# Optimization experiments

Measured on AMD Instinct MI355X. Metric: run time of the kernel, lower is better.

Reference implementation:

```python
import jax, jax.numpy as jnp
import numpy as np

B, T, H, D = 1, 2048, 32, 64
SCALE = 0.015625  # 1/64 = 1/head_size
DEG = 2


def setup_inputs() -> dict:
    key = jax.random.key(0)
    k1, k2, k3, k4 = jax.random.split(key, 4)
    q = jax.random.normal(k1, (B, T, H, D), dtype=jnp.float32)
    k = jax.random.normal(k2, (B, T, H, D), dtype=jnp.float32)
    v = jax.random.normal(k3, (B, T, H, D), dtype=jnp.float32)
    # log_G: per-token, per-head log decay (must be <= 0)
    g = -0.1 * jax.random.uniform(k4, (B, T, H), dtype=jnp.float32)
    return {"q": q, "k": k, "v": v, "g": g}


def reference(q, k, v, g):
    # q,k,v: [B,T,H,D]; g: [B,T,H] log-decay (log_G)
    # Power retention, deg=2, attention (quadratic) form for T <= switch_over_seq_len.
    g_cum = jnp.cumsum(g, axis=1)                         # [B,T,H]
    gc = jnp.transpose(g_cum, (0, 2, 1))                  # [B,H,T]
    # decay weight exp(gc[t]-gc[s]) for s<=t, 0 otherwise
    log_decay = gc[:, :, :, None] - gc[:, :, None, :]     # [B,H,T,S]
    causal = jnp.tril(jnp.ones((T, T), dtype=bool))
    decay = jnp.where(causal, jnp.exp(log_decay), 0.0)    # [B,H,T,S]
    qk = jnp.einsum("bthd,bshd->bhts", q, k) * SCALE      # [B,H,T,S]
    w = (qk ** DEG) * decay                               # nonneg scores, deg=2
    num = jnp.einsum("bhts,bshd->bthd", w, v)             # [B,T,H,D]
    denom = jnp.transpose(w.sum(-1), (0, 2, 1))           # [B,T,H]
    out = num / jnp.maximum(denom, 1.0)[..., None]
    return out
```

## Files before the change

kernel.cpp:

```cpp
#include <hip/hip_runtime.h>

#define T_DIM 2048
#define H_DIM 32
#define D_DIM 64
#define SCALE_F 0.015625f
#define TILE_STRIDE 2048

typedef unsigned short ushort;
typedef __attribute__((ext_vector_type(8))) short short8;
typedef __attribute__((ext_vector_type(16))) float f32x16;
typedef __attribute__((ext_vector_type(2))) float f32x2;
typedef __attribute__((ext_vector_type(4))) float f32x4;

#define MFMA32(A, B, C) __builtin_amdgcn_mfma_f32_32x32x16_bf16((A), (B), (C), 0, 0, 0)

__global__ __launch_bounds__(256)
void cumsum_g_kernel(const float* __restrict__ g, float* __restrict__ gc) {
    const int h = blockIdx.x;
    const int tid = threadIdx.x;
    const int PER = T_DIM / 256;

    __shared__ float sums[256];

    float loc[8];
    float run = 0.f;
    const int t0 = tid * PER;
    for (int i = 0; i < PER; ++i) {
        run += g[(size_t)(t0 + i) * H_DIM + h];
        loc[i] = run;
    }
    sums[tid] = run;
    __syncthreads();

    for (int off = 1; off < 256; off <<= 1) {
        float vv = (tid >= off) ? sums[tid - off] : 0.f;
        __syncthreads();
        sums[tid] += vv;
        __syncthreads();
    }
    float excl = (tid == 0) ? 0.f : sums[tid - 1];

    for (int i = 0; i < PER; ++i)
        gc[(size_t)h * T_DIM + t0 + i] = excl + loc[i];
}

__device__ __forceinline__ ushort f2bf(float x) {
    unsigned u = __float_as_uint(x);
    unsigned r = (u + 0x7fffu + ((u >> 16) & 1u)) >> 16;
    return (ushort)r;
}

__global__ __launch_bounds__(256)
void prep_kernel(const float* __restrict__ q, const float* __restrict__ k,
                 const float* __restrict__ v, const float* __restrict__ gc,
                 ushort* __restrict__ qfrag, ushort* __restrict__ kfrag,
                 ushort* __restrict__ vfrag) {
    __shared__ ushort qt_l[64 * 64];
    __shared__ ushort kt_l[64 * 64];

    const int h   = blockIdx.x;
    const int tt  = blockIdx.y;
    const int tid = threadIdx.x;

    {
        const int r    = tid >> 2;
        const int dseg = (tid & 3) * 16;
        const int t    = tt * 64 + r;
        const float gct = gc[(size_t)h * T_DIM + t];
        const float eq = SCALE_F * __expf(0.5f * gct);
        const float ek = __expf(-0.5f * gct);
        const float* qp = q + ((size_t)t * H_DIM + h) * 64 + dseg;
        const float* kp = k + ((size_t)t * H_DIM + h) * 64 + dseg;
        union { ushort u[16]; uint4 uu[2]; } oq, ok;
#pragma unroll
        for (int i = 0; i < 16; ++i) {
            oq.u[i] = f2bf(qp[i] * eq);
            ok.u[i] = f2bf(kp[i] * ek);
        }
        const int c0 = (tid & 3) * 2;
#pragma unroll
        for (int cc = 0; cc < 2; ++cc) {
            const int slot = (c0 + cc) ^ (r & 7);
            *reinterpret_cast<uint4*>(&qt_l[r * 64 + slot * 8]) = oq.uu[cc];
            *reinterpret_cast<uint4*>(&kt_l[r * 64 + slot * 8]) = ok.uu[cc];
        }
    }
    __syncthreads();

#pragma unroll
    for (int n = 0; n < 2; ++n) {
        const int ch   = tid + 256 * n;
        const int l31  = ch & 31;
        const int hi   = (ch >> 5) & 1;
        const int ks   = (ch >> 6) & 3;
        const int t32r = ch >> 8;
        const int row  = t32r * 32 + l31;
        const int slot = (2 * ks + hi) ^ (row & 7);
        uint4 qq = *reinterpret_cast<const uint4*>(&qt_l[row * 64 + slot * 8]);
        uint4 kk = *reinterpret_cast<const uint4*>(&kt_l[row * 64 + slot * 8]);
        const size_t base = ((size_t)h * 64 + tt * 2 + t32r) * TILE_STRIDE
                          + (size_t)(((ks * 2 + hi) * 32) + l31) * 8;
        *reinterpret_cast<uint4*>(qfrag + base) = qq;
        *reinterpret_cast<uint4*>(kfrag + base) = kk;
    }

#pragma unroll
    for (int n = 0; n < 2; ++n) {
        const int c9   = (tid >> 5) + 8 * n;
        const int l31  = tid & 31;
        const int hi   = c9 & 1;
        const int kh2  = (c9 >> 1) & 1;
        const int dblk = (c9 >> 2) & 1;
        const int s32r = c9 >> 3;
        const int tb = tt * 64 + s32r * 32 + kh2 * 16 + hi * 8;
        union { ushort u[8]; uint4 uu; } ov;
#pragma unroll
        for (int j = 0; j < 8; ++j)
            ov.u[j] = f2bf(v[((size_t)(tb + j) * H_DIM + h) * 64 + dblk * 32 + l31]);
        const size_t base = ((size_t)h * 64 + tt * 2 + s32r) * TILE_STRIDE
                          + (size_t)((((dblk * 2 + kh2) * 2 + hi) * 32) + l31) * 8;
        *reinterpret_cast<uint4*>(vfrag + base) = ov.uu;
    }
}

__device__ __forceinline__ short8 ld8(const ushort* p) {
    return *reinterpret_cast<const short8*>(p);
}

__device__ __forceinline__ unsigned cvt_pk_bf16(float lo, float hi) {
    unsigned r;
    asm("v_cvt_pk_bf16_f32 %0, %1, %2" : "=v"(r) : "v"(lo), "v"(hi));
    return r;
}

__device__ __forceinline__ short8 pack_w2(const f32x2* w2) {
    unsigned p0 = cvt_pk_bf16(w2[0][0], w2[0][1]);
    unsigned p1 = cvt_pk_bf16(w2[1][0], w2[1][1]);
    unsigned p2 = cvt_pk_bf16(w2[2][0], w2[2][1]);
    unsigned p3 = cvt_pk_bf16(w2[3][0], w2[3][1]);
    asm("v_permlane32_swap_b32 %0, %1" : "+v"(p0), "+v"(p2));
    asm("v_permlane32_swap_b32 %0, %1" : "+v"(p1), "+v"(p3));
    union { unsigned u[4]; short8 s; } af;
    af.u[0] = p0; af.u[1] = p1; af.u[2] = p2; af.u[3] = p3;
    return af.s;
}

template<int MODE>
__device__ __forceinline__ void unitD(
    const ushort* __restrict__ kb, const ushort* __restrict__ vb,
    int lofs, int hi, int l31,
    const short8 (&qr)[4], f32x16& o0, f32x16& o1, f32x2& den2)
{
    const short8 kf0 = ld8(kb + lofs);
    const short8 kf1 = ld8(kb + 512 + lofs);
    const short8 kf2 = ld8(kb + 1024 + lofs);
    const short8 kf3 = ld8(kb + 1536 + lofs);
    const short8 vf0 = ld8(vb + lofs);
    const short8 vf1 = ld8(vb + 512 + lofs);
    const short8 vf2 = ld8(vb + 1024 + lofs);
    const short8 vf3 = ld8(vb + 1536 + lofs);

    f32x16 c;
#pragma unroll
    for (int i = 0; i < 16; ++i) c[i] = 0.f;
    c = MFMA32(kf0, qr[0], c);
    c = MFMA32(kf1, qr[1], c);
    c = MFMA32(kf2, qr[2], c);
    c = MFMA32(kf3, qr[3], c);

    f32x2 w2[8];
#pragma unroll
    for (int i = 0; i < 8; ++i) {
        const int r0 = 2 * i;
        f32x2 x; x[0] = c[r0]; x[1] = c[r0 + 1];
        f32x2 ww = x * x;
        if (MODE == 1) {
            const int sl0 = (r0 & 3) + 8 * (r0 >> 2) + 4 * hi;
            ww[0] = (sl0 <= l31) ? ww[0] : 0.f;
            ww[1] = (sl0 + 1 <= l31) ? ww[1] : 0.f;
        }
        w2[i] = ww;
        den2 += ww;
    }
    const short8 a0 = pack_w2(&w2[0]);
    o0 = MFMA32(a0, vf0, o0);
    o1 = MFMA32(a0, vf2, o1);
    const short8 a1 = pack_w2(&w2[4]);
    o0 = MFMA32(a1, vf1, o0);
    o1 = MFMA32(a1, vf3, o1);
}

__global__ __launch_bounds__(256, 4)
void retention_main_kernel(const ushort* __restrict__ qfrag,
                           const ushort* __restrict__ kfrag,
                           const ushort* __restrict__ vfrag,
                           float* __restrict__ out) {
    __shared__ float lds_o[2][32][64];
    __shared__ float lds_d[2][32];

    const int bid  = blockIdx.x;
    const int h    = bid & 31;
    const int pair = bid >> 5;
    const int tid  = threadIdx.x;
    const int w    = tid >> 6;
    const int lane = tid & 63;
    const int hi   = lane >> 5;
    const int l31  = lane & 31;
    const int lofs = hi * 256 + l31 * 8;

    const int m   = (w < 2) ? (63 - pair) : pair;
    const int par = w & 1;

    short8 qr[4];
    {
        const ushort* qb = qfrag + ((size_t)h * 64 + m) * TILE_STRIDE;
#pragma unroll
        for (int ks = 0; ks < 4; ++ks) qr[ks] = ld8(qb + ks * 512 + lofs);
    }

    f32x16 o0, o1;
#pragma unroll
    for (int i = 0; i < 16; ++i) { o0[i] = 0.f; o1[i] = 0.f; }
    f32x2 d2; d2[0] = 0.f; d2[1] = 0.f;

    const ushort* khb = kfrag + (size_t)h * 64 * TILE_STRIDE;
    const ushort* vhb = vfrag + (size_t)h * 64 * TILE_STRIDE;

    int st = par;
    for (; st < m; st += 2)
        unitD<0>(khb + (size_t)st * TILE_STRIDE, vhb + (size_t)st * TILE_STRIDE,
                 lofs, hi, l31, qr, o0, o1, d2);
    if (st == m)
        unitD<1>(khb + (size_t)m * TILE_STRIDE, vhb + (size_t)m * TILE_STRIDE,
                 lofs, hi, l31, qr, o0, o1, d2);

    float den = d2[0] + d2[1];
    den += __shfl_xor(den, 32);

    const int slot = w >> 1;
    if (par == 1) {
#pragma unroll
        for (int rr = 0; rr < 16; ++rr) {
            const int row = (rr & 3) + 8 * (rr >> 2) + 4 * hi;
            lds_o[slot][row][l31]      = o0[rr];
            lds_o[slot][row][32 + l31] = o1[rr];
        }
        if (hi == 0) lds_d[slot][l31] = den;
    }
    __syncthreads();
    if (par == 0) {
        const float dtot = den + lds_d[slot][l31];
#pragma unroll
        for (int rr = 0; rr < 16; ++rr) {
            const int row = (rr & 3) + 8 * (rr >> 2) + 4 * hi;
            const float s0 = o0[rr] + lds_o[slot][row][l31];
            const float s1 = o1[rr] + lds_o[slot][row][32 + l31];
            const float dt = __shfl(dtot, row);
            const float inv = 1.f / fmaxf(dt, 1.f);
            const int t = m * 32 + row;
            float* op = out + ((size_t)t * H_DIM + h) * 64;
            op[l31]      = s0 * inv;
            op[32 + l31] = s1 * inv;
        }
    }
}

extern "C" void kernel_launch(void* const* d_in, const int* in_sizes, int n_in,
                              void* d_out, int out_size, void* d_ws, size_t ws_size,
                              hipStream_t stream) {
    const float* q = (const float*)d_in[0];
    const float* k = (const float*)d_in[1];
    const float* v = (const float*)d_in[2];
    const float* g = (const float*)d_in[3];
    float* out = (float*)d_out;

    const size_t GC_BYTES = (size_t)H_DIM * T_DIM * sizeof(float);
    const size_t BF_ELEMS = (size_t)H_DIM * T_DIM * D_DIM;

    float* gc = (float*)d_ws;
    ushort* qfrag = (ushort*)((char*)d_ws + GC_BYTES);
    ushort* kfrag = qfrag + BF_ELEMS;
    ushort* vfrag = kfrag + BF_ELEMS;

    cumsum_g_kernel<<<H_DIM, 256, 0, stream>>>(g, gc);
    prep_kernel<<<dim3(H_DIM, T_DIM / 64), 256, 0, stream>>>(q, k, v, gc,
                                                             qfrag, kfrag, vfrag);
    retention_main_kernel<<<1024, 256, 0, stream>>>(qfrag, kfrag, vfrag, out);
}
```

Measured before the change: 52.48 us.

## Give each wave its own query tile instead of splitting key tiles across wave pairs

Each wave now owns a full 32-row query tile and walks all of its key tiles alone. Waves are paired so one takes a tile from the top of the causal triangle and one from the bottom, which keeps the work per block balanced. This removes the LDS reduction between wave pairs and the __syncthreads, and halves the grid to 512 blocks. Launch bounds drop to 2 blocks per CU. The trade-off is a longer serial chain per wave and fewer blocks to spread across the CUs.

```diff
diff --git a/kernel.cpp b/kernel.cpp
--- a/kernel.cpp
+++ b/kernel.cpp
@@ -190,17 +190,14 @@
     o1 = MFMA32(a1, vf3, o1);
 }
 
-__global__ __launch_bounds__(256, 4)
+__global__ __launch_bounds__(256, 2)
 void retention_main_kernel(const ushort* __restrict__ qfrag,
                            const ushort* __restrict__ kfrag,
                            const ushort* __restrict__ vfrag,
                            float* __restrict__ out) {
-    __shared__ float lds_o[2][32][64];
-    __shared__ float lds_d[2][32];
-
     const int bid  = blockIdx.x;
     const int h    = bid & 31;
-    const int pair = bid >> 5;
+    const int p    = bid >> 5;
     const int tid  = threadIdx.x;
     const int w    = tid >> 6;
     const int lane = tid & 63;
@@ -208,8 +205,10 @@
     const int l31  = lane & 31;
     const int lofs = hi * 256 + l31 * 8;
 
-    const int m   = (w < 2) ? (63 - pair) : pair;
-    const int par = w & 1;
+    const int m = (w == 0) ? (62 - 2 * p)
+                : (w == 1) ? (63 - 2 * p)
+                : (w == 2) ? (2 * p)
+                :            (2 * p + 1);
 
     short8 qr[4];
     {
@@ -226,42 +225,31 @@
     const ushort* khb = kfrag + (size_t)h * 64 * TILE_STRIDE;
     const ushort* vhb = vfrag + (size_t)h * 64 * TILE_STRIDE;
 
-    int st = par;
-    for (; st < m; st += 2)
+    int st = 0;
+    for (; st + 1 < m; st += 2) {
         unitD<0>(khb + (size_t)st * TILE_STRIDE, vhb + (size_t)st * TILE_STRIDE,
                  lofs, hi, l31, qr, o0, o1, d2);
-    if (st == m)
-        unitD<1>(khb + (size_t)m * TILE_STRIDE, vhb + (size_t)m * TILE_STRIDE,
+        unitD<0>(khb + (size_t)(st + 1) * TILE_STRIDE, vhb + (size_t)(st + 1) * TILE_STRIDE,
                  lofs, hi, l31, qr, o0, o1, d2);
+    }
+    if (st < m)
+        unitD<0>(khb + (size_t)st * TILE_STRIDE, vhb + (size_t)st * TILE_STRIDE,
+                 lofs, hi, l31, qr, o0, o1, d2);
+    unitD<1>(khb + (size_t)m * TILE_STRIDE, vhb + (size_t)m * TILE_STRIDE,
+             lofs, hi, l31, qr, o0, o1, d2);
 
     float den = d2[0] + d2[1];
     den += __shfl_xor(den, 32);
 
-    const int slot = w >> 1;
-    if (par == 1) {
-#pragma unroll
-        for (int rr = 0; rr < 16; ++rr) {
-            const int row = (rr & 3) + 8 * (rr >> 2) + 4 * hi;
-            lds_o[slot][row][l31]      = o0[rr];
-            lds_o[slot][row][32 + l31] = o1[rr];
-        }
-        if (hi == 0) lds_d[slot][l31] = den;
-    }
-    __syncthreads();
-    if (par == 0) {
-        const float dtot = den + lds_d[slot][l31];
-#pragma unroll
-        for (int rr = 0; rr < 16; ++rr) {
-            const int row = (rr & 3) + 8 * (rr >> 2) + 4 * hi;
-            const float s0 = o0[rr] + lds_o[slot][row][l31];
-            const float s1 = o1[rr] + lds_o[slot][row][32 + l31];
-            const float dt = __shfl(dtot, row);
-            const float inv = 1.f / fmaxf(dt, 1.f);
-            const int t = m * 32 + row;
-            float* op = out + ((size_t)t * H_DIM + h) * 64;
-            op[l31]      = s0 * inv;
-            op[32 + l31] = s1 * inv;
-        }
+#pragma unroll
+    for (int rr = 0; rr < 16; ++rr) {
+        const int row = (rr & 3) + 8 * (rr >> 2) + 4 * hi;
+        const float dt = __shfl(den, row);
+        const float inv = 1.f / fmaxf(dt, 1.f);
+        const int t = m * 32 + row;
+        float* op = out + ((size_t)t * H_DIM + h) * 64;
+        op[l31]      = o0[rr] * inv;
+        op[32 + l31] = o1[rr] * inv;
     }
 }
 
@@ -285,5 +273,5 @@
     cumsum_g_kernel<<<H_DIM, 256, 0, stream>>>(g, gc);
     prep_kernel<<<dim3(H_DIM, T_DIM / 64), 256, 0, stream>>>(q, k, v, gc,
                                                              qfrag, kfrag, vfrag);
-    retention_main_kernel<<<1024, 256, 0, stream>>>(qfrag, kfrag, vfrag, out);
-}
+    retention_main_kernel<<<512, 256, 0, stream>>>(qfrag, kfrag, vfrag, out);
+}
```

Result: slower. 68.19 us (+29.9%).
